# Performance work log

Hardware: AMD Instinct MI355X
Metric: run time of the kernel (lower is better)

The kernel has to match this reference:

```python
import jax
import jax.numpy as jnp
import numpy as np
from jax import lax

NUM_TAGS = 24
BATCH = 8192
SEQ_LEN = 512


def setup_inputs() -> dict:
    key = jax.random.key(0)
    k1, k2 = jax.random.split(key)
    inputs = jax.random.normal(k1, (BATCH, SEQ_LEN, NUM_TAGS), dtype=jnp.float32)
    # glorot_uniform for (num_tags, num_tags)
    limit = float(np.sqrt(6.0 / (NUM_TAGS + NUM_TAGS)))
    transitions = jax.random.uniform(
        k2, (NUM_TAGS, NUM_TAGS), dtype=jnp.float32, minval=-limit, maxval=limit
    )
    return {"inputs": inputs, "transitions": transitions}


def _viterbi_decode(potentials, transitions):
    """Linear-chain CRF Viterbi decode (full-length sequences).

    potentials: [B, T, K] unary scores; transitions: [K, K] (prev -> cur).
    Returns int32 tag sequence [B, T].
    """
    emissions = jnp.swapaxes(potentials, 0, 1)  # [T, B, K]

    def fwd(alpha, emit_t):
        # scores[b, i, j] = alpha[b, i] + transitions[i, j]
        scores = alpha[:, :, None] + transitions[None, :, :]  # [B, K, K]
        bp = jnp.argmax(scores, axis=1).astype(jnp.int32)      # [B, K] best prev tag
        alpha_new = jnp.max(scores, axis=1) + emit_t            # [B, K]
        return alpha_new, bp

    alpha_T, bps = lax.scan(fwd, emissions[0], emissions[1:])  # bps: [T-1, B, K]
    last_tag = jnp.argmax(alpha_T, axis=-1).astype(jnp.int32)  # [B]

    def bwd(tag_next, bp_t):
        # bp_t[b, tag_next[b]] = best tag at step t given tag at t+1
        tag_t = jnp.take_along_axis(bp_t, tag_next[:, None], axis=1)[:, 0]
        return tag_t, tag_t

    _, tags_prefix = lax.scan(bwd, last_tag, bps, reverse=True)  # [T-1, B]
    tags = jnp.concatenate([tags_prefix, last_tag[None, :]], axis=0)  # [T, B]
    return jnp.swapaxes(tags, 0, 1)  # [B, T]


def reference(inputs, transitions):
    # Inference path of CRF.call: Viterbi decode then one-hot encode.
    viterbi = _viterbi_decode(inputs, transitions)            # [B, T] int32
    return jax.nn.one_hot(viterbi, NUM_TAGS, dtype=inputs.dtype)  # [B, T, K]
```

## Files before the change

### kernel.cpp

```cpp
#include <hip/hip_runtime.h>
#include <stdint.h>

#define B 8192
#define T 512
#define K 24

__device__ __forceinline__ float max3f(float a, float b, float c) {
    return fmaxf(fmaxf(a, b), c);
}

__global__ __launch_bounds__(64) __attribute__((amdgpu_waves_per_eu(2, 2)))
void crf_forward(const float* __restrict__ inp,
                 const float* __restrict__ trans,
                 float* __restrict__ out)
{
    __shared__ float alpha[2][4][K];

    const int lane = threadIdx.x;
    const int grp  = lane >> 4;
    const int l    = lane & 15;
    const bool act = (l < 12);
    const int c0   = act ? 2 * l : 22;
    const int b    = blockIdx.x * 4 + grp;

    float tc[2][K];
#pragma unroll
    for (int j = 0; j < 2; ++j)
#pragma unroll
        for (int i = 0; i < K; ++i) tc[j][i] = trans[i * K + c0 + j];

    const float* ebl = inp + (size_t)b * T * K + c0;
    float*       obl = out + (size_t)b * T * K + c0;

    float* a0 = &alpha[0][grp][0];
    float* a1 = &alpha[1][grp][0];

    {
        float2 x = *(const float2*)(ebl);
        if (act) {
            a0[c0] = x.x; a0[c0 + 1] = x.y;
            *(float2*)(obl) = x;
        }
    }

    float2 eA = *(const float2*)(ebl + 1 * K);
    float2 eB = *(const float2*)(ebl + 2 * K);
    float2 eC = *(const float2*)(ebl + 3 * K);
    float2 eD = *(const float2*)(ebl + 4 * K);

#define STEP(AC, AN, E, TT) do {                                              \
    float a_[K];                                                              \
    _Pragma("unroll")                                                         \
    for (int c = 0; c < 6; ++c) {                                             \
        float4 v_ = ((const float4*)(AC))[c];                                 \
        a_[4*c] = v_.x; a_[4*c+1] = v_.y; a_[4*c+2] = v_.z; a_[4*c+3] = v_.w; \
    }                                                                         \
    float r_[2];                                                              \
    _Pragma("unroll")                                                         \
    for (int j = 0; j < 2; ++j) {                                             \
        float u_[8];                                                          \
        _Pragma("unroll")                                                     \
        for (int k = 0; k < 8; ++k)                                           \
            u_[k] = max3f(a_[3*k]   + tc[j][3*k],                             \
                          a_[3*k+1] + tc[j][3*k+1],                           \
                          a_[3*k+2] + tc[j][3*k+2]);                          \
        float w0_ = max3f(u_[0], u_[1], u_[2]);                               \
        float w1_ = max3f(u_[3], u_[4], u_[5]);                               \
        float w2_ = fmaxf(u_[6], u_[7]);                                      \
        r_[j] = max3f(w0_, w1_, w2_);                                         \
    }                                                                         \
    float o0_ = r_[0] + (E).x, o1_ = r_[1] + (E).y;                           \
    if (act) {                                                                \
        (AN)[c0] = o0_; (AN)[c0 + 1] = o1_;                                   \
        float2 st_; st_.x = o0_; st_.y = o1_;                                 \
        *(float2*)(obl + (size_t)(TT) * K) = st_;                             \
    }                                                                         \
} while (0)

#pragma unroll 1
    for (int ch = 0; ch < 127; ++ch) {
        const int t = 1 + 4 * ch;
        float2 nA = *(const float2*)(ebl + (size_t)(t + 4) * K);
        float2 nB = *(const float2*)(ebl + (size_t)(t + 5) * K);
        float2 nC = *(const float2*)(ebl + (size_t)(t + 6) * K);
        int t7 = t + 7; t7 = t7 > 511 ? 511 : t7;
        float2 nD = *(const float2*)(ebl + (size_t)t7 * K);

        STEP(a0, a1, eA, t);
        STEP(a1, a0, eB, t + 1);
        STEP(a0, a1, eC, t + 2);
        STEP(a1, a0, eD, t + 3);

        eA = nA; eB = nB; eC = nC; eD = nD;
    }
    STEP(a0, a1, eA, 509);
    STEP(a1, a0, eB, 510);
    STEP(a0, a1, eC, 511);
#undef STEP
}

__device__ __forceinline__ float groupmax32(float v) {
    float t;
    t = __int_as_float(__builtin_amdgcn_mov_dpp(__float_as_int(v), 0xB1, 0xF, 0xF, true));
    v = fmaxf(v, t);
    t = __int_as_float(__builtin_amdgcn_mov_dpp(__float_as_int(v), 0x4E, 0xF, 0xF, true));
    v = fmaxf(v, t);
    t = __int_as_float(__builtin_amdgcn_mov_dpp(__float_as_int(v), 0x141, 0xF, 0xF, true));
    v = fmaxf(v, t);
    t = __int_as_float(__builtin_amdgcn_mov_dpp(__float_as_int(v), 0x140, 0xF, 0xF, true));
    v = fmaxf(v, t);
    t = __int_as_float(__builtin_amdgcn_ds_swizzle(__float_as_int(v), 0x401F));
    v = fmaxf(v, t);
    return v;
}

__global__ __launch_bounds__(256) __attribute__((amdgpu_waves_per_eu(4, 4)))
void crf_backtrack(const float* __restrict__ trans,
                   float* __restrict__ out)
{
    __shared__ float tl[K * 25];

    const int tid = threadIdx.x;
    for (int idx = tid; idx < K * K; idx += 256) {
        int i = idx / K, j = idx - K * i;
        tl[i * 25 + j] = trans[idx];
    }
    __syncthreads();

    const int lane = tid & 63;
    const int half = lane >> 5;
    const int i    = lane & 31;
    const int wv   = tid >> 6;
    const int b    = blockIdx.x * 8 + wv * 2 + half;
    const int shmt = half * 32;

    const bool act = (i < K);
    const int  io  = act ? i : (K - 1);

    float* ob = out + (size_t)b * T * K;
    const float* rp  = ob + (size_t)511 * K + io;
    float*       wpp = ob + (size_t)511 * K + io;

    float q[8];
#pragma unroll
    for (int s = 0; s < 8; ++s) { q[7 - s] = *rp; rp -= K; }

    int cur;
    {
        float s = act ? q[7] : -INFINITY;
        float M = groupmax32(s);
        uint32_t m32 = (uint32_t)(__ballot(s == M) >> shmt);
        cur = (int)__builtin_ctz(m32);
        if (act) *wpp = (i == cur) ? 1.0f : 0.0f;
        wpp -= K;
        q[7] = *rp; rp -= K;
    }

#define STEP_BT(S, TT) do {                                                   \
    float tv_ = tl[io * 25 + cur];                                            \
    float s_  = act ? (q[S] + tv_) : -INFINITY;                               \
    float M_  = groupmax32(s_);                                               \
    uint32_t m32_ = (uint32_t)(__ballot(s_ == M_) >> shmt);                   \
    cur = (int)__builtin_ctz(m32_);                                           \
    if (act) *wpp = (i == cur) ? 1.0f : 0.0f;                                 \
    wpp -= K;                                                                 \
    if ((TT) >= 8) { q[S] = *rp; rp -= K; }                                   \
} while (0)

#pragma unroll 1
    for (int it = 0; it < 63; ++it) {
        const int t0 = 510 - 8 * it;
        STEP_BT(6, t0);     STEP_BT(5, t0 - 1);
        STEP_BT(4, t0 - 2); STEP_BT(3, t0 - 3);
        STEP_BT(2, t0 - 4); STEP_BT(1, t0 - 5);
        STEP_BT(0, t0 - 6); STEP_BT(7, t0 - 7);
    }
    STEP_BT(6, 6); STEP_BT(5, 5); STEP_BT(4, 4);
    STEP_BT(3, 3); STEP_BT(2, 2); STEP_BT(1, 1); STEP_BT(0, 0);
#undef STEP_BT
}

extern "C" void kernel_launch(void* const* d_in, const int* in_sizes, int n_in,
                              void* d_out, int out_size, void* d_ws, size_t ws_size,
                              hipStream_t stream) {
    const float* inp   = (const float*)d_in[0];
    const float* trans = (const float*)d_in[1];
    float*       out   = (float*)d_out;

    crf_forward<<<B / 4, 64, 0, stream>>>(inp, trans, out);
    crf_backtrack<<<B / 8, 256, 0, stream>>>(trans, out);
}
```

Baseline: 352.8 us.

## Replace LDS alpha exchange with DPP/swizzle cross-lane broadcast in forward Viterbi

The forward recurrence no longer stages alpha through shared memory each step. Each 16-lane group now exchanges alpha pairs in registers using DPP row rotates and ds_swizzle, and the transition columns are pre-permuted to match the shuffled lane order, with duplicated padding lanes. This removes the LDS write/read round trip on the serial critical path. In exchange it adds about 14 cross-lane ops per step and does 32 instead of 24 add/max candidates.

```diff
diff --git a/kernel.cpp b/kernel.cpp
--- a/kernel.cpp
+++ b/kernel.cpp
@@ -7,6 +7,66 @@
 
 __device__ __forceinline__ float max3f(float a, float b, float c) {
     return fmaxf(fmaxf(a, b), c);
+}
+
+#define ROR8(v) __builtin_amdgcn_mov_dpp((v), 0x128, 0xF, 0xF, true)
+#define XG4(v)  __builtin_amdgcn_ds_swizzle((v), 0x101F)
+#define D2x(v)  __builtin_amdgcn_mov_dpp((v), 0x4E, 0xF, 0xF, true)
+#define D1x(v)  __builtin_amdgcn_mov_dpp((v), 0xB1, 0xF, 0xF, true)
+
+__device__ __forceinline__ void vstep(float& n0, float& n1,
+                                      float e0, float e1,
+                                      const float (&tcr)[2][32],
+                                      float* gp, bool act)
+{
+    const int i0 = __float_as_int(n0), i1 = __float_as_int(n1);
+    const int r0 = ROR8(i0), r1 = ROR8(i1);
+    const int f0 = XG4(i0), f1 = XG4(i1), f2 = XG4(r0), f3 = XG4(r1);
+
+    int pa[8], pb[8];
+    pa[0] = i0;      pb[0] = i1;
+    pa[1] = r0;      pb[1] = r1;
+    pa[2] = f0;      pb[2] = f1;
+    pa[3] = f2;      pb[3] = f3;
+    pa[4] = D2x(i0); pb[4] = D2x(i1);
+    pa[5] = D2x(r0); pb[5] = D2x(r1);
+    pa[6] = D2x(f0); pb[6] = D2x(f1);
+    pa[7] = D2x(f2); pb[7] = D2x(f3);
+
+    float s[32];
+#pragma unroll
+    for (int p = 0; p < 8; ++p) {
+        s[4*p+0] = __int_as_float(pa[p]);
+        s[4*p+1] = __int_as_float(pb[p]);
+        s[4*p+2] = __int_as_float(D1x(pa[p]));
+        s[4*p+3] = __int_as_float(D1x(pb[p]));
+    }
+
+    float r[2];
+#pragma unroll
+    for (int j = 0; j < 2; ++j) {
+        float q[32];
+#pragma unroll
+        for (int i = 0; i < 32; ++i) q[i] = s[i] + tcr[j][i];
+        float v0 = max3f(q[0],  q[1],  q[2]);
+        float v1 = max3f(q[3],  q[4],  q[5]);
+        float v2 = max3f(q[6],  q[7],  q[8]);
+        float v3 = max3f(q[9],  q[10], q[11]);
+        float v4 = max3f(q[12], q[13], q[14]);
+        float v5 = max3f(q[15], q[16], q[17]);
+        float v6 = max3f(q[18], q[19], q[20]);
+        float v7 = max3f(q[21], q[22], q[23]);
+        float v8 = max3f(q[24], q[25], q[26]);
+        float v9 = max3f(q[27], q[28], q[29]);
+        float vA = fmaxf(q[30], q[31]);
+        float w0 = max3f(v0, v1, v2);
+        float w1 = max3f(v3, v4, v5);
+        float w2 = max3f(v6, v7, v8);
+        float w3 = fmaxf(v9, vA);
+        r[j] = fmaxf(max3f(w0, w1, w2), w3);
+    }
+    n0 = r[0] + e0; n1 = r[1] + e1;
+    if (act) { float2 st; st.x = n0; st.y = n1; *(float2*)gp = st; }
 }
 
 __global__ __launch_bounds__(64) __attribute__((amdgpu_waves_per_eu(2, 2)))
@@ -14,68 +74,45 @@
                  const float* __restrict__ trans,
                  float* __restrict__ out)
 {
-    __shared__ float alpha[2][4][K];
-
     const int lane = threadIdx.x;
-    const int grp  = lane >> 4;
+    const int g    = lane >> 4;
     const int l    = lane & 15;
     const bool act = (l < 12);
-    const int c0   = act ? 2 * l : 22;
-    const int b    = blockIdx.x * 4 + grp;
-
-    float tc[2][K];
-#pragma unroll
-    for (int j = 0; j < 2; ++j)
-#pragma unroll
-        for (int i = 0; i < K; ++i) tc[j][i] = trans[i * K + c0 + j];
+    const int  lx  = act ? l : 11;
+    const int  c0  = 2 * lx;
+    const int  b   = blockIdx.x * 4 + g;
+
+    const int MP[8] = {0, 8, 4, 12, 2, 10, 6, 14};
+    float tcr[2][32];
+#pragma unroll
+    for (int p = 0; p < 8; ++p) {
+        const int ma = (l ^ MP[p]) & 15;
+        const int mb = ma ^ 1;
+        const int ra = 2 * (ma < 11 ? ma : 11);
+        const int rb = 2 * (mb < 11 ? mb : 11);
+#pragma unroll
+        for (int j = 0; j < 2; ++j) {
+            tcr[j][4*p+0] = trans[(ra + 0) * K + c0 + j];
+            tcr[j][4*p+1] = trans[(ra + 1) * K + c0 + j];
+            tcr[j][4*p+2] = trans[(rb + 0) * K + c0 + j];
+            tcr[j][4*p+3] = trans[(rb + 1) * K + c0 + j];
+        }
+    }
 
     const float* ebl = inp + (size_t)b * T * K + c0;
     float*       obl = out + (size_t)b * T * K + c0;
 
-    float* a0 = &alpha[0][grp][0];
-    float* a1 = &alpha[1][grp][0];
-
+    float n0, n1;
     {
         float2 x = *(const float2*)(ebl);
-        if (act) {
-            a0[c0] = x.x; a0[c0 + 1] = x.y;
-            *(float2*)(obl) = x;
-        }
+        n0 = x.x; n1 = x.y;
+        if (act) *(float2*)(obl) = x;
     }
 
     float2 eA = *(const float2*)(ebl + 1 * K);
     float2 eB = *(const float2*)(ebl + 2 * K);
     float2 eC = *(const float2*)(ebl + 3 * K);
     float2 eD = *(const float2*)(ebl + 4 * K);
-
-#define STEP(AC, AN, E, TT) do {                                              \
-    float a_[K];                                                              \
-    _Pragma("unroll")                                                         \
-    for (int c = 0; c < 6; ++c) {                                             \
-        float4 v_ = ((const float4*)(AC))[c];                                 \
-        a_[4*c] = v_.x; a_[4*c+1] = v_.y; a_[4*c+2] = v_.z; a_[4*c+3] = v_.w; \
-    }                                                                         \
-    float r_[2];                                                              \
-    _Pragma("unroll")                                                         \
-    for (int j = 0; j < 2; ++j) {                                             \
-        float u_[8];                                                          \
-        _Pragma("unroll")                                                     \
-        for (int k = 0; k < 8; ++k)                                           \
-            u_[k] = max3f(a_[3*k]   + tc[j][3*k],                             \
-                          a_[3*k+1] + tc[j][3*k+1],                           \
-                          a_[3*k+2] + tc[j][3*k+2]);                          \
-        float w0_ = max3f(u_[0], u_[1], u_[2]);                               \
-        float w1_ = max3f(u_[3], u_[4], u_[5]);                               \
-        float w2_ = fmaxf(u_[6], u_[7]);                                      \
-        r_[j] = max3f(w0_, w1_, w2_);                                         \
-    }                                                                         \
-    float o0_ = r_[0] + (E).x, o1_ = r_[1] + (E).y;                           \
-    if (act) {                                                                \
-        (AN)[c0] = o0_; (AN)[c0 + 1] = o1_;                                   \
-        float2 st_; st_.x = o0_; st_.y = o1_;                                 \
-        *(float2*)(obl + (size_t)(TT) * K) = st_;                             \
-    }                                                                         \
-} while (0)
 
 #pragma unroll 1
     for (int ch = 0; ch < 127; ++ch) {
@@ -86,18 +123,22 @@
         int t7 = t + 7; t7 = t7 > 511 ? 511 : t7;
         float2 nD = *(const float2*)(ebl + (size_t)t7 * K);
 
-        STEP(a0, a1, eA, t);
-        STEP(a1, a0, eB, t + 1);
-        STEP(a0, a1, eC, t + 2);
-        STEP(a1, a0, eD, t + 3);
+        vstep(n0, n1, eA.x, eA.y, tcr, obl + (size_t)(t    ) * K, act);
+        vstep(n0, n1, eB.x, eB.y, tcr, obl + (size_t)(t + 1) * K, act);
+        vstep(n0, n1, eC.x, eC.y, tcr, obl + (size_t)(t + 2) * K, act);
+        vstep(n0, n1, eD.x, eD.y, tcr, obl + (size_t)(t + 3) * K, act);
 
         eA = nA; eB = nB; eC = nC; eD = nD;
     }
-    STEP(a0, a1, eA, 509);
-    STEP(a1, a0, eB, 510);
-    STEP(a0, a1, eC, 511);
-#undef STEP
-}
+    vstep(n0, n1, eA.x, eA.y, tcr, obl + (size_t)509 * K, act);
+    vstep(n0, n1, eB.x, eB.y, tcr, obl + (size_t)510 * K, act);
+    vstep(n0, n1, eC.x, eC.y, tcr, obl + (size_t)511 * K, act);
+}
+
+#undef ROR8
+#undef XG4
+#undef D2x
+#undef D1x
 
 __device__ __forceinline__ float groupmax32(float v) {
     float t;
```

Result: slower. 443.4 us (+25.7%).
